# Kernel optimization log

Hardware: AMD Instinct MI355X
Metric: run time of the kernel (lower is better)

The kernel has to match this reference:

```python
import jax, jax.numpy as jnp
import numpy as np

B = 1024          # batch of positions
K = 64            # king squares
F = 640           # 64 squares * 10 piece types
C = 256           # accumulator channels


def setup_inputs() -> dict:
    key = jax.random.key(0)
    k1, k2, k3 = jax.random.split(key, 3)
    piece_positions = jax.random.randint(k1, (B, 64, 10), 0, 2).astype(jnp.bool_)
    king_positions = jax.random.randint(k2, (B, 2), 0, K, dtype=jnp.int32)
    input_weights = jax.random.normal(k3, (K, F + 1, C), dtype=jnp.float32)
    bias = jnp.zeros((C,), dtype=jnp.float32)
    return {
        "piece_positions": piece_positions,
        "king_positions": king_positions,
        "input_weights": input_weights,
        "bias": bias,
    }


def reference(piece_positions, king_positions, input_weights, bias):
    # Flatten the (64, 10) boolean piece plane into 640 HalfKP features.
    b = piece_positions.shape[0]
    p = piece_positions.reshape(b, F).astype(input_weights.dtype)          # (B, 640)
    # Gather each sample's white/black king weight slabs: (B, 2, 641, 256)
    Wg = jnp.take(input_weights, king_positions, axis=0)
    # Sparse-feature sum for both halves, contracted over feature dim and
    # summed over the two king perspectives in one einsum.
    halves = jnp.einsum("bf,bsfc->bc", p, Wg[:, :, :F, :])                 # (B, 256)
    extra = Wg[:, :, F, :].sum(axis=1)                                     # row 640 for each king
    return halves + extra + bias
```

## Files before the change

### kernel.cpp

```cpp
#include <hip/hip_runtime.h>
#include <hip/hip_bf16.h>


#define F_DIM 640
#define C_DIM 256
#define SLAB_STRIDE (641 * 256)
#define NKING 64
#define LCAP 256
#define NC_MAX 64

#define WS_MASK_OFF 0
#define WS_PART_OFF 81920
#define WS_NEED (WS_PART_OFF + 2 * 1024 * 256 * 4)

typedef float  f32x4  __attribute__((ext_vector_type(4)));
typedef short  bf16x8 __attribute__((ext_vector_type(8)));

__device__ __forceinline__ bf16x8 mk_a8(unsigned m32, int g) {
    const unsigned by = (m32 >> (g * 8)) & 0xFFu;
    union { unsigned u[4]; bf16x8 v; } r;
    #pragma unroll
    for (int i = 0; i < 4; ++i)
        r.u[i] = (((by >> (2 * i)) & 1u) ? 0x3F80u : 0u) |
                 (((by >> (2 * i + 1)) & 1u) ? 0x3F800000u : 0u);
    return r.v;
}

__device__ __forceinline__ f32x4 do_win(const float* __restrict__ Wc,
                                        unsigned m32, int g, int ks, f32x4 acc) {
    float wt[8];
    #pragma unroll
    for (int j = 0; j < 8; ++j)
        wt[j] = Wc[(size_t)(ks * 32 + g * 8 + j) * C_DIM];
    union { unsigned u[4]; bf16x8 v; } bb;
    #pragma unroll
    for (int j = 0; j < 4; ++j)
        asm("v_cvt_pk_bf16_f32 %0, %1, %2"
            : "=v"(bb.u[j]) : "v"(wt[2 * j]), "v"(wt[2 * j + 1]));
    const bf16x8 af = mk_a8(m32, g);
    return __builtin_amdgcn_mfma_f32_16x16x32_bf16(af, bb.v, acc, 0, 0, 0);
}

__global__ __launch_bounds__(256)
void pack_masks(const int* __restrict__ pieces,
                unsigned long long* __restrict__ mask,
                int nwords)
{
    const int gw = blockIdx.x * 4 + (threadIdx.x >> 6);
    const int lane = threadIdx.x & 63;
    if (gw >= nwords) return;
    const int v = pieces[(size_t)gw * 64 + lane];
    const unsigned long long m = __ballot(v != 0);
    if (lane == 0) mask[gw] = m;
}

__global__ __launch_bounds__(512, 4)
void halfkp_mfma(const float* __restrict__ W,
                 const unsigned long long* __restrict__ mask,
                 const int* __restrict__ kings,
                 float* __restrict__ partial,
                 int nent)
{
    const int k  = blockIdx.x;
    const int cq = blockIdx.y;
    const int t  = threadIdx.x;
    const int wv = t >> 6, lane = t & 63;
    const int mt  = wv & 1;
    const int ntc = (wv >> 1) & 1;
    const int kh  = wv >> 2;
    const int li = lane & 15, g = lane >> 4;
    const int col = cq * 32 + ntc * 16 + li;

    __shared__ int s_ent[LCAP];
    __shared__ int s_cb[NC_MAX + 1];
    __shared__ unsigned s_m32[32][21];
    __shared__ f32x4 s_red[4][64];
    __shared__ int s_nk;

    {
        const int NC = nent >> 6;
        const int nit = NC >> 3;
        unsigned long long mm[8];
        #pragma unroll
        for (int it = 0; it < 8; ++it) {
            if (it < nit) {
                const int c = wv + (it << 3);
                const int kk = kings[(c << 6) + lane];
                mm[it] = __ballot(kk == k);
                if (lane == 0) s_cb[c] = (int)__popcll(mm[it]);
            }
        }
        __syncthreads();
        if (t == 0) {
            int s = 0;
            for (int c = 0; c < NC; ++c) { const int v = s_cb[c]; s_cb[c] = s; s += v; }
            s_nk = min(s, LCAP);
        }
        __syncthreads();
        const unsigned long long lt = (1ull << lane) - 1ull;
        #pragma unroll
        for (int it = 0; it < 8; ++it) {
            if (it < nit) {
                const int c = wv + (it << 3);
                if ((mm[it] >> lane) & 1ull) {
                    const int pos = s_cb[c] + (int)__popcll(mm[it] & lt);
                    if (pos < LCAP) s_ent[pos] = (c << 6) + lane;
                }
            }
        }
        __syncthreads();
    }
    const int n_k = s_nk;

    const float* __restrict__ Wc = W + (size_t)k * SLAB_STRIDE + col;

    for (int mb = 0; mb < n_k; mb += 32) {
        const int nc = min(n_k - mb, 32);

        for (int idx = t; idx < 32 * 21; idx += 512) {
            const int row = idx & 31, ks = idx >> 5;
            const int id = (row < nc) ? s_ent[mb + row] : -1;
            unsigned v = 0;
            if (id >= 0) {
                if (ks < 20) {
                    const unsigned long long mw = mask[(size_t)(id >> 1) * 10 + (ks >> 1)];
                    v = (unsigned)(mw >> ((ks & 1) * 32));
                } else {
                    v = 1u;
                }
            }
            s_m32[row][ks] = v;
        }
        __syncthreads();

        const unsigned* mrow = s_m32[mt * 16 + li];
        f32x4 acc = {0.f, 0.f, 0.f, 0.f};
        if (kh == 0) {
            #pragma unroll 2
            for (int ks = 0; ks < 10; ++ks)
                acc = do_win(Wc, mrow[ks], g, ks, acc);
        } else {
            #pragma unroll 2
            for (int ks = 10; ks < 20; ++ks)
                acc = do_win(Wc, mrow[ks], g, ks, acc);
            {
                const float w640 = Wc[(size_t)F_DIM * C_DIM];
                unsigned pk;
                asm("v_cvt_pk_bf16_f32 %0, %1, %2" : "=v"(pk) : "v"(w640), "v"(w640));
                union { unsigned u[4]; bf16x8 v; } bb;
                bb.u[0] = bb.u[1] = bb.u[2] = bb.u[3] = pk;
                const bf16x8 af = mk_a8(mrow[20], g);
                acc = __builtin_amdgcn_mfma_f32_16x16x32_bf16(af, bb.v, acc, 0, 0, 0);
            }
            s_red[wv & 3][lane] = acc;
        }
        __syncthreads();
        if (kh == 0) {
            acc += s_red[wv & 3][lane];
            #pragma unroll
            for (int i = 0; i < 4; ++i) {
                const int row = mt * 16 + 4 * g + i;
                if (row < nc) {
                    const int id = s_ent[mb + row];
                    partial[(((size_t)(id & 1)) * 1024 + (id >> 1)) * C_DIM + col] = acc[i];
                }
            }
        }
        __syncthreads();
    }
}

__global__ __launch_bounds__(256)
void finalize(const float* __restrict__ partial,
              const float* __restrict__ bias,
              float* __restrict__ out)
{
    const int i = blockIdx.x * 256 + threadIdx.x;
    const float4 b4 = ((const float4*)bias)[i & 63];
    const float4 p0 = ((const float4*)partial)[i];
    const float4 p1 = ((const float4*)partial)[1024 * 64 + i];
    float4 o;
    o.x = b4.x + p0.x + p1.x;
    o.y = b4.y + p0.y + p1.y;
    o.z = b4.z + p0.z + p1.z;
    o.w = b4.w + p0.w + p1.w;
    ((float4*)out)[i] = o;
}

__global__ __launch_bounds__(256)
void halfkp_fallback(const int* __restrict__ pieces, const int* __restrict__ kings,
                     const float* __restrict__ W, const float* __restrict__ bias,
                     float* __restrict__ out)
{
    const int b = blockIdx.x;
    const int c = threadIdx.x;
    const int lane = c & 63;
    const int k0 = kings[2 * b + 0];
    const int k1 = kings[2 * b + 1];
    const float* W0 = W + (size_t)k0 * SLAB_STRIDE + c;
    const float* W1 = W + (size_t)k1 * SLAB_STRIDE + c;
    float acc = bias[c] + W0[640 * 256] + W1[640 * 256];
    const int* pi = pieces + (size_t)b * F_DIM;
    #pragma unroll
    for (int ch = 0; ch < 10; ++ch) {
        int v = pi[ch * 64 + lane];
        unsigned long long m = __ballot(v != 0);
        const float* b0 = W0 + ch * 64 * 256;
        const float* b1 = W1 + ch * 64 * 256;
        while (m) {
            const int f = __builtin_ctzll(m);
            m &= m - 1;
            acc += b0[f * 256] + b1[f * 256];
        }
    }
    out[(size_t)b * C_DIM + c] = acc;
}

extern "C" void kernel_launch(void* const* d_in, const int* in_sizes, int n_in,
                              void* d_out, int out_size, void* d_ws, size_t ws_size,
                              hipStream_t stream) {
    const int* pieces = (const int*)d_in[0];
    const int* kings  = (const int*)d_in[1];
    const float* W    = (const float*)d_in[2];
    const float* bias = (const float*)d_in[3];
    float* out        = (float*)d_out;

    const int B = in_sizes[1] / 2;
    const int nent = 2 * B;
    const int nwords = B * 10;

    if (ws_size < (size_t)WS_NEED) {
        halfkp_fallback<<<dim3(B), dim3(C_DIM), 0, stream>>>(pieces, kings, W, bias, out);
        return;
    }

    unsigned long long* mask = (unsigned long long*)((char*)d_ws + WS_MASK_OFF);
    float* part = (float*)((char*)d_ws + WS_PART_OFF);

    pack_masks<<<dim3((nwords + 3) / 4), dim3(256), 0, stream>>>(pieces, mask, nwords);
    halfkp_mfma<<<dim3(NKING, 8), dim3(512), 0, stream>>>(W, mask, kings, part, nent);
    finalize<<<dim3(B * 64 / 256), dim3(256), 0, stream>>>(part, bias, out);
}
```

Measured before the change: 28.00 us.

## Stage bf16 weight slab in LDS and fuse mask packing into main kernel

Each block now loads its king's 641x32 weight slice once, converts it to packed bf16 pairs, and keeps it in padded shared memory. MFMA windows then read operands from LDS instead of re-fetching global weights for every 32-entry batch. The separate pack_masks kernel is gone: the main kernel ballots the piece planes directly for the entries it needs, which saves one launch. In exchange every block pays an up-front weight load even when it has few or no entries, and the shared-memory footprint grows to about 44KB, which may limit occupancy.

```diff
diff --git a/kernel.cpp b/kernel.cpp
--- a/kernel.cpp
+++ b/kernel.cpp
@@ -8,13 +8,21 @@
 #define NKING 64
 #define LCAP 256
 #define NC_MAX 64
-
-#define WS_MASK_OFF 0
-#define WS_PART_OFF 81920
-#define WS_NEED (WS_PART_OFF + 2 * 1024 * 256 * 4)
+#define WPAD 33
+
+#define WS_PART_OFF 0
+#define WS_NEED (2 * 1024 * 256 * 4)
 
 typedef float  f32x4  __attribute__((ext_vector_type(4)));
 typedef short  bf16x8 __attribute__((ext_vector_type(8)));
+
+__device__ __forceinline__ unsigned f2bf_pk(float a, float b) {
+    union { float f; unsigned u; } x, y;
+    x.f = a; y.f = b;
+    const unsigned ra = (x.u + 0x7FFFu + ((x.u >> 16) & 1u)) >> 16;
+    const unsigned rb = (y.u + 0x7FFFu + ((y.u >> 16) & 1u)) >> 16;
+    return (ra & 0xFFFFu) | (rb << 16);
+}
 
 __device__ __forceinline__ bf16x8 mk_a8(unsigned m32, int g) {
     const unsigned by = (m32 >> (g * 8)) & 0xFFu;
@@ -26,37 +34,9 @@
     return r.v;
 }
 
-__device__ __forceinline__ f32x4 do_win(const float* __restrict__ Wc,
-                                        unsigned m32, int g, int ks, f32x4 acc) {
-    float wt[8];
-    #pragma unroll
-    for (int j = 0; j < 8; ++j)
-        wt[j] = Wc[(size_t)(ks * 32 + g * 8 + j) * C_DIM];
-    union { unsigned u[4]; bf16x8 v; } bb;
-    #pragma unroll
-    for (int j = 0; j < 4; ++j)
-        asm("v_cvt_pk_bf16_f32 %0, %1, %2"
-            : "=v"(bb.u[j]) : "v"(wt[2 * j]), "v"(wt[2 * j + 1]));
-    const bf16x8 af = mk_a8(m32, g);
-    return __builtin_amdgcn_mfma_f32_16x16x32_bf16(af, bb.v, acc, 0, 0, 0);
-}
-
-__global__ __launch_bounds__(256)
-void pack_masks(const int* __restrict__ pieces,
-                unsigned long long* __restrict__ mask,
-                int nwords)
-{
-    const int gw = blockIdx.x * 4 + (threadIdx.x >> 6);
-    const int lane = threadIdx.x & 63;
-    if (gw >= nwords) return;
-    const int v = pieces[(size_t)gw * 64 + lane];
-    const unsigned long long m = __ballot(v != 0);
-    if (lane == 0) mask[gw] = m;
-}
-
 __global__ __launch_bounds__(512, 4)
 void halfkp_mfma(const float* __restrict__ W,
-                 const unsigned long long* __restrict__ mask,
+                 const int* __restrict__ pieces,
                  const int* __restrict__ kings,
                  float* __restrict__ partial,
                  int nent)
@@ -69,8 +49,10 @@
     const int ntc = (wv >> 1) & 1;
     const int kh  = wv >> 2;
     const int li = lane & 15, g = lane >> 4;
-    const int col = cq * 32 + ntc * 16 + li;
-
+    const int colL = ntc * 16 + li;
+    const int colG = cq * 32 + colL;
+
+    __shared__ unsigned s_W[336 * WPAD];
     __shared__ int s_ent[LCAP];
     __shared__ int s_cb[NC_MAX + 1];
     __shared__ unsigned s_m32[32][21];
@@ -112,48 +94,62 @@
     }
     const int n_k = s_nk;
 
-    const float* __restrict__ Wc = W + (size_t)k * SLAB_STRIDE + col;
+    {
+        const float* __restrict__ Wq = W + (size_t)k * SLAB_STRIDE + cq * 32;
+        const int c = t & 31;
+        const int r0 = t >> 5;
+        #pragma unroll 3
+        for (int it = 0; it < 21; ++it) {
+            const int fp = it * 16 + r0;
+            const int fe = min(2 * fp, F_DIM);
+            const int fo = min(2 * fp + 1, F_DIM);
+            const float we = Wq[(size_t)fe * C_DIM + c];
+            const float wo = Wq[(size_t)fo * C_DIM + c];
+            s_W[fp * WPAD + c] = f2bf_pk(we, wo);
+        }
+    }
 
     for (int mb = 0; mb < n_k; mb += 32) {
         const int nc = min(n_k - mb, 32);
 
-        for (int idx = t; idx < 32 * 21; idx += 512) {
-            const int row = idx & 31, ks = idx >> 5;
-            const int id = (row < nc) ? s_ent[mb + row] : -1;
-            unsigned v = 0;
+        #pragma unroll
+        for (int j = 0; j < 4; ++j) {
+            const int r = wv + 8 * j;
+            const int id = (r < nc) ? s_ent[mb + r] : -1;
             if (id >= 0) {
-                if (ks < 20) {
-                    const unsigned long long mw = mask[(size_t)(id >> 1) * 10 + (ks >> 1)];
-                    v = (unsigned)(mw >> ((ks & 1) * 32));
-                } else {
-                    v = 1u;
+                const int* __restrict__ pb = pieces + (size_t)(id >> 1) * F_DIM;
+                #pragma unroll 2
+                for (int w2 = 0; w2 < 10; ++w2) {
+                    const unsigned long long m64 = __ballot(pb[w2 * 64 + lane] != 0);
+                    if (lane == 0) {
+                        s_m32[r][2 * w2]     = (unsigned)m64;
+                        s_m32[r][2 * w2 + 1] = (unsigned)(m64 >> 32);
+                    }
                 }
-            }
-            s_m32[row][ks] = v;
+                if (lane == 0) s_m32[r][20] = 1u;
+            } else {
+                if (lane < 21) s_m32[r][lane] = 0u;
+            }
         }
         __syncthreads();
 
         const unsigned* mrow = s_m32[mt * 16 + li];
         f32x4 acc = {0.f, 0.f, 0.f, 0.f};
-        if (kh == 0) {
+        {
+            const int ks_beg = kh ? 10 : 0;
+            const int ks_end = kh ? 21 : 10;
             #pragma unroll 2
-            for (int ks = 0; ks < 10; ++ks)
-                acc = do_win(Wc, mrow[ks], g, ks, acc);
-        } else {
-            #pragma unroll 2
-            for (int ks = 10; ks < 20; ++ks)
-                acc = do_win(Wc, mrow[ks], g, ks, acc);
-            {
-                const float w640 = Wc[(size_t)F_DIM * C_DIM];
-                unsigned pk;
-                asm("v_cvt_pk_bf16_f32 %0, %1, %2" : "=v"(pk) : "v"(w640), "v"(w640));
+            for (int ks = ks_beg; ks < ks_end; ++ks) {
+                const unsigned* bp = &s_W[(ks * 16 + g * 4) * WPAD + colL];
                 union { unsigned u[4]; bf16x8 v; } bb;
-                bb.u[0] = bb.u[1] = bb.u[2] = bb.u[3] = pk;
-                const bf16x8 af = mk_a8(mrow[20], g);
+                #pragma unroll
+                for (int jj = 0; jj < 4; ++jj)
+                    bb.u[jj] = bp[jj * WPAD];
+                const bf16x8 af = mk_a8(mrow[ks], g);
                 acc = __builtin_amdgcn_mfma_f32_16x16x32_bf16(af, bb.v, acc, 0, 0, 0);
             }
-            s_red[wv & 3][lane] = acc;
-        }
+        }
+        if (kh == 1) s_red[wv & 3][lane] = acc;
         __syncthreads();
         if (kh == 0) {
             acc += s_red[wv & 3][lane];
@@ -162,7 +158,7 @@
                 const int row = mt * 16 + 4 * g + i;
                 if (row < nc) {
                     const int id = s_ent[mb + row];
-                    partial[(((size_t)(id & 1)) * 1024 + (id >> 1)) * C_DIM + col] = acc[i];
+                    partial[(((size_t)(id & 1)) * 1024 + (id >> 1)) * C_DIM + colG] = acc[i];
                 }
             }
         }
@@ -227,17 +223,14 @@
 
     const int B = in_sizes[1] / 2;
     const int nent = 2 * B;
-    const int nwords = B * 10;
 
     if (ws_size < (size_t)WS_NEED) {
         halfkp_fallback<<<dim3(B), dim3(C_DIM), 0, stream>>>(pieces, kings, W, bias, out);
         return;
     }
 
-    unsigned long long* mask = (unsigned long long*)((char*)d_ws + WS_MASK_OFF);
     float* part = (float*)((char*)d_ws + WS_PART_OFF);
 
-    pack_masks<<<dim3((nwords + 3) / 4), dim3(256), 0, stream>>>(pieces, mask, nwords);
-    halfkp_mfma<<<dim3(NKING, 8), dim3(512), 0, stream>>>(W, mask, kings, part, nent);
+    halfkp_mfma<<<dim3(NKING, 8), dim3(512), 0, stream>>>(W, pieces, kings, part, nent);
     finalize<<<dim3(B * 64 / 256), dim3(256), 0, stream>>>(part, bias, out);
 }
```

After: 38.41 us. 1.37x slower.
